# Kernel optimization log

Hardware: AMD Instinct MI355X
Metric: run time of the kernel (lower is better)

Reference implementation:

```python
import jax, jax.numpy as jnp
import numpy as np

# NOTE: VectorDiscoBlock / VectorDotProduct source was not provided; this is a
# faithful structural reconstruction of the local-support DISCO spherical conv:
# kernel_shape radial bases psi_r plus 2 polarized (tangential/radial, i.e.
# curl-like/div-like) vector bases, with paths W_ss, W_vs, W_sv, W_vv, W_vs2
# (flux-form scalar*vector products), pointwise_ss, sv_product (scalar times
# identity/rotated vector) and the physics weight initialization copied exactly
# from _init_physics_weights. All weights are constants (requires_grad=False),
# so they are contracted with the basis stencils once into effective spatial
# conv kernels.

RE = 6371000.0; RGAS = 287.0; CP = 1004.0; OMEGA_E = 7.292e-05
K_LEV = 3; NK = 6; NS = K_LEV * NK + 1; NV = K_LEV
B, H, W = 2, 256, 512
KS = 5   # number of radial kernel bases (kernel_shape)
S = 5    # spatial stencil extent
T_ANOM, KE, ZETA, DIV, TK, QK = 0, 1, 2, 3, 4, 5

def _ch(l, k):
    return l * NK + k

def _conv(x, k, groups=1):
    # zero pad lat (axis 2), circular pad lon (axis 3)
    p = k.shape[-1] // 2
    x = jnp.pad(x, ((0, 0), (0, 0), (p, p), (0, 0)))
    x = jnp.concatenate([x[..., -p:], x, x[..., :p]], axis=-1)
    return jax.lax.conv_general_dilated(
        x, k, (1, 1), 'VALID',
        dimension_numbers=('NCHW', 'OIHW', 'NCHW'),
        feature_group_count=groups)

def _build_params():
    # radial scalar bases psi[r,h,w]; polarized vector bases Vb[r,pol,h,w,comp]
    yy, xx = np.meshgrid(np.arange(S) - S // 2, np.arange(S) - S // 2, indexing='ij')
    rr = np.sqrt(yy ** 2 + xx ** 2)
    centers = np.linspace(0.0, 2.0, KS)
    psi = np.maximum(0.0, 1.0 - np.abs(rr[None] - centers[:, None, None]))
    psi = psi / psi.sum((1, 2), keepdims=True)
    inv = np.where(rr > 0, 1.0 / np.maximum(rr, 1e-9), 0.0)
    er = np.stack([yy * inv, xx * inv], -1)    # radial (div-like) polarization
    et = np.stack([-xx * inv, yy * inv], -1)   # tangential (curl-like)
    Vb = np.stack([et[None] * psi[..., None], er[None] * psi[..., None]], 1)
    # pressure levels: log-spaced 1e5 -> 1e4 Pa (default)
    p = np.array([1e5 * np.exp(-k * np.log(10.0) / (K_LEV - 1)) for k in range(K_LEV)])
    lpr = np.log(p[:-1] / p[1:])
    p_lo = np.concatenate([p[:1], 0.5 * (p[:-1] + p[1:])])
    p_up = np.concatenate([0.5 * (p[:-1] + p[1:]), [0.0]])
    delta_p = p_lo - p_up
    # physics weights (exact copy of _init_physics_weights)
    W_ss = np.zeros((NS, NS, KS)); W_vs = np.zeros((NS, NV, KS, 2))
    W_sv = np.zeros((NV, NS, KS, 2)); W_vv = np.zeros((NV, NV, KS, 2))
    W_vs2 = np.zeros((NS, NV, KS, 2))
    for k in range(K_LEV):
        W_vs[_ch(k, ZETA), k, :, 0] = 1.0 / RE
        W_vs[_ch(k, DIV), k, :, 1] = 1.0 / RE
    for ko in range(K_LEV):
        for ki in range(ko):
            W_sv[ko, _ch(ki, T_ANOM), :, 1] = -RGAS * lpr[ki] / RE
        W_sv[ko, _ch(ko, KE), :, 1] = -1.0 / RE
    for k in range(K_LEV):
        W_vs2[_ch(k, TK), k, :, 1] = -1.0 / RE
        W_vs2[_ch(k, QK), k, :, 1] = -1.0 / RE
    nu = 1.0e5  # diffusion_coeff
    lap_w = np.array([-4.0, 1.0, 0.5, 0.25, 0.125]) * (nu / RE ** 2)
    for k in range(K_LEV):
        W_ss[_ch(k, TK), _ch(k, TK)] = lap_w
        W_ss[_ch(k, QK), _ch(k, QK)] = lap_w
        W_vv[k, k, :, 0] = lap_w
    pw_ss = np.zeros((NS, NS)); pw_ss[K_LEV * NK, K_LEV * NK] = 1.0
    svp = np.zeros((NS, NV, 2))
    for k in range(K_LEV):
        svp[_ch(k, ZETA), k, 1] = 1.0
    svp[K_LEV * NK, :, 1] = -1.0
    ke_w = 0.5 * np.eye(K_LEV)
    # contract constant weights with bases -> effective spatial conv kernels
    eye2 = np.eye(2); eps2 = np.array([[0.0, -1.0], [1.0, 0.0]])
    k_ss = np.einsum('oir,rhw->oihw', W_ss, psi)
    k_vs = np.einsum('oirp,rphwc->oichw', W_vs, Vb).reshape(NS, NV * 2, S, S)
    k_sv = np.einsum('oirp,rphwc->ocihw', W_sv, Vb).reshape(NV * 2, NS, S, S)
    k_vv = (np.einsum('oir,rhw,ab->oaibhw', W_vv[..., 0], psi, eye2)
            + np.einsum('oir,rhw,ab->oaibhw', W_vv[..., 1], psi, eps2)).reshape(NV * 2, NV * 2, S, S)
    k_vs2 = np.einsum('oirp,rphwc->oichw', W_vs2, Vb).reshape(NS, NV * 2, S, S)
    lats = np.linspace(np.pi / 2, -np.pi / 2, H)
    f_cor = (2.0 * OMEGA_E * np.sin(lats)).reshape(1, 1, H, 1)
    f32 = lambda a: jnp.asarray(a, jnp.float32)
    return dict(k_ss=f32(k_ss), k_vs=f32(k_vs), k_sv=f32(k_sv), k_vv=f32(k_vv),
                k_vs2=f32(k_vs2), pw_ss=f32(pw_ss), svp=f32(svp), ke_w=f32(ke_w),
                f_cor=f32(f_cor), p_lev=f32(p), delta_p=f32(delta_p))

def _step(uv, T, q, k_ss, k_vs, k_sv, k_vv, k_vs2, pw_ss, svp, ke_w,
          f_cor, p_lev, delta_p, dt):
    Bq, Kl, Hh, Ww = T.shape

    def _tend(uv, T, q):
        # VectorDotProduct: ke[b,o] = sum_i w[o,i] * (uv_i . uv_i)
        ke = jnp.einsum('oi,bihwc,bihwc->bohw', ke_w, uv, uv)
        T_anom = T - T.mean(axis=(-2, -1), keepdims=True)
        z = jnp.zeros_like(T)
        per = jnp.stack([T_anom, ke, z, z, T, q], axis=2).reshape(Bq, Kl * NK, Hh, Ww)
        x_s = jnp.concatenate(
            [per, jnp.broadcast_to(f_cor, (Bq, 1, Hh, Ww)).astype(T.dtype)], axis=1)
        xv_vc = jnp.moveaxis(uv, -1, 2)                 # [B,K,2,H,W]
        xv = xv_vc.reshape(Bq, Kl * 2, Hh, Ww)
        # flux-form scalar*vector product fields for W_vs2 (grouped by scalar ch)
        prod = (x_s[:, :, None, None] * xv_vc[:, None]).reshape(Bq, NS * Kl * 2, Hh, Ww)
        y_s = (_conv(x_s, k_ss) + _conv(xv, k_vs)
               + _conv(prod, k_vs2, groups=NS)
               + jnp.einsum('oi,bihw->bohw', pw_ss, x_s))
        yv = _conv(x_s, k_sv) + _conv(xv, k_vv)
        y_v = jnp.moveaxis(yv.reshape(Bq, Kl, 2, Hh, Ww), 2, -1)
        # sv_product: scalar * (identity | rotated) vector
        a0 = jnp.einsum('sv,bshw->bvhw', svp[..., 0], x_s)
        a1 = jnp.einsum('sv,bshw->bvhw', svp[..., 1], x_s)
        rot = jnp.stack([-uv[..., 1], uv[..., 0]], axis=-1)
        y_v = y_v + a0[..., None] * uv + a1[..., None] * rot
        ysl = y_s[:, :Kl * NK].reshape(Bq, Kl, NK, Hh, Ww)
        div, dT, dq = ysl[:, :, DIV], ysl[:, :, TK], ysl[:, :, QK]
        # omega integrated upward from surface (cumsum over levels)
        oh = jnp.concatenate(
            [jnp.zeros((Bq, 1, Hh, Ww), T.dtype),
             jnp.cumsum(div * delta_p[None, :, None, None], axis=1)], axis=1)
        omega = 0.5 * (oh[:, :-1] + oh[:, 1:])
        pk = p_lev[None, :, None, None]
        dTdp = jnp.concatenate([
            (T[:, 1:2] - T[:, 0:1]) / (p_lev[1] - p_lev[0]),
            (T[:, 2:] - T[:, :-2]) / (p_lev[2:] - p_lev[:-2])[None, :, None, None],
            (T[:, -1:] - T[:, -2:-1]) / (p_lev[-1] - p_lev[-2])], axis=1)
        dT = dT + omega * ((RGAS / CP) * T / pk - dTdp)
        return y_v, dT, dq

    dtf = float(dt)
    k1 = _tend(uv, T, q)
    k2 = _tend(uv + 0.5 * dtf * k1[0], T + 0.5 * dtf * k1[1], q + 0.5 * dtf * k1[2])
    k3 = _tend(uv + 0.5 * dtf * k2[0], T + 0.5 * dtf * k2[1], q + 0.5 * dtf * k2[2])
    k4 = _tend(uv + dtf * k3[0], T + dtf * k3[1], q + dtf * k3[2])
    c = dtf / 6.0
    return (uv + c * (k1[0] + 2 * k2[0] + 2 * k3[0] + k4[0]),
            T + c * (k1[1] + 2 * k2[1] + 2 * k3[1] + k4[1]),
            q + c * (k1[2] + 2 * k2[2] + 2 * k3[2] + k4[2]))

def setup_inputs() -> dict:
    key = jax.random.key(0)
    k1, k2, k3 = jax.random.split(key, 3)
    inp = dict(
        uv=jax.random.normal(k1, (B, K_LEV, H, W, 2), jnp.float32),
        T=jax.random.normal(k2, (B, K_LEV, H, W), jnp.float32),
        q=jax.random.normal(k3, (B, K_LEV, H, W), jnp.float32),
    )
    inp.update(_build_params())
    inp['dt'] = 120
    return inp

def reference(uv, T, q, k_ss, k_vs, k_sv, k_vv, k_vs2, pw_ss, svp, ke_w,
              f_cor, p_lev, delta_p, dt):
    return _step(uv, T, q, k_ss, k_vs, k_sv, k_vv, k_vs2, pw_ss, svp, ke_w,
                 f_cor, p_lev, delta_p, dt)
```

## Files before the change

kernel.cpp:

```cpp
#include <hip/hip_runtime.h>

#define HH 256
#define WW 512
#define BQ 2
#define HWQ (HH*WW)
#define TW 68
#define TH 12
#define CSTR 64
#define TRL 20

#define RGASC 287.0f
#define CPC   1004.0f

typedef float f32x4 __attribute__((ext_vector_type(4)));
typedef short s16x8 __attribute__((ext_vector_type(8)));

static __device__ uint4 g_Wm[25*64];
static __device__ float g_FC[HH*16];
static __device__ float g_S [HH*3*16];
static __device__ float g_part[2][6*512];
static __device__ float g_uvs[BQ*3*HWQ*2];
static __device__ float g_Ts [BQ*3*HWQ];
static __device__ float g_qs [BQ*3*HWQ];
static __device__ float g_aT [BQ*3*HWQ];
static __device__ float g_aq [BQ*3*HWQ];
static __device__ float g_auv[BQ*3*HWQ*2];


__device__ __forceinline__ unsigned short f2bf(float f) {
  unsigned int u = __builtin_bit_cast(unsigned int, f);
  u += 0x7fffu + ((u >> 16) & 1u);
  return (unsigned short)(u >> 16);
}
__device__ __forceinline__ float bflo(unsigned int d) {
  return __builtin_bit_cast(float, d << 16);
}
__device__ __forceinline__ float bfhi(unsigned int d) {
  return __builtin_bit_cast(float, d & 0xffff0000u);
}
__device__ __forceinline__ int foMap(int o) {
  return (o < 3) ? 6*o + 3 : (o < 6) ? 6*(o-3) + 4 : 6*(o-6) + 5;
}

__global__ __launch_bounds__(256) void prelude_kernel(
    const float* __restrict__ T0,
    const float* __restrict__ k_ss, const float* __restrict__ k_vs,
    const float* __restrict__ k_sv, const float* __restrict__ k_vv,
    const float* __restrict__ k_vs2, const float* __restrict__ f_cor)
{
  if (blockIdx.x < 3072) {
    int bk = blockIdx.x >> 9, chunk = blockIdx.x & 511;
    float v = T0[bk*HWQ + chunk*256 + threadIdx.x];
    int l = threadIdx.x & 63, w = threadIdx.x >> 6;
    #pragma unroll
    for (int off=32; off; off >>= 1) v += __shfl_down(v, off);
    __shared__ float sr[4];
    if (l == 0) sr[w] = v;
    __syncthreads();
    if (threadIdx.x == 0) g_part[0][bk*512 + chunk] = sr[0]+sr[1]+sr[2]+sr[3];
    return;
  }
  int tid = (blockIdx.x - 3072)*256 + threadIdx.x;
  if (tid < 1600) {
    int l = tid & 63, t = tid >> 6;
    int o = l & 15, g = l >> 4;
    int dy = t/5, dx = t%5;
    unsigned short h[8];
    #pragma unroll
    for (int e=0;e<8;++e) {
      int s = 8*g + e; float val = 0.f;
      if (o < 15) {
        int fo = foMap(o), vo = o - 9;
        if (s < 12) {
          int k = s >> 2, c4 = s & 3;
          if (c4 >= 2) {
            int j = 2*k + (c4-2);
            val = (o<9) ? k_vs[((fo*6+j)*5+dy)*5+dx]
                        : k_vv[((vo*6+j)*5+dy)*5+dx];
          } else {
            int ifull = 6*k + ((c4==0) ? 4 : 5);
            val = (o<9) ? k_ss[((fo*19+ifull)*5+dy)*5+dx]
                        : k_sv[((vo*19+ifull)*5+dy)*5+dx];
            if (c4 == 0) {
              int ia = 6*k;
              val += (o<9) ? k_ss[((fo*19+ia)*5+dy)*5+dx]
                           : k_sv[((vo*19+ia)*5+dy)*5+dx];
            }
          }
        } else if (s < 15) {
          int ifull = 6*(s-12) + 1;
          val = (o<9) ? k_ss[((fo*19+ifull)*5+dy)*5+dx]
                      : k_sv[((vo*19+ifull)*5+dy)*5+dx];
        } else if (s >= 16 && s < 22) {
          int k = (s-16)>>1, c = (s-16)&1;
          if (o == 3+k) val = k_vs2[(((6*k+4)*6 + 2*k+c)*5+dy)*5+dx];
        } else if (s >= 22 && s < 28) {
          int k = (s-22)>>1, c = (s-22)&1;
          if (o == 6+k) val = k_vs2[(((6*k+5)*6 + 2*k+c)*5+dy)*5+dx];
        }
      }
      h[e] = f2bf(val);
    }
    uint4 wv;
    wv.x = h[0] | ((unsigned)h[1]<<16);  wv.y = h[2] | ((unsigned)h[3]<<16);
    wv.z = h[4] | ((unsigned)h[5]<<16);  wv.w = h[6] | ((unsigned)h[7]<<16);
    g_Wm[tid] = wv;
  } else if (tid < 1600 + HH*16) {
    int e = tid - 1600;
    int o = e & 15, r = e >> 4;
    float val = 0.f;
    if (o < 15) {
      int fo = foMap(o), vo = o - 9;
      for (int t=0;t<25;++t) {
        int dy = t/5, dx = t%5;
        int ar = r + dy - 2;
        if (ar < 0 || ar >= HH) continue;
        float f = f_cor[ar];
        float wv = (o<9) ? k_ss[((fo*19+18)*5+dy)*5+dx]
                         : k_sv[((vo*19+18)*5+dy)*5+dx];
        val += wv * f;
      }
    }
    g_FC[e] = val;
  } else if (tid < 1600 + HH*16 + HH*3*16) {
    int e = tid - 1600 - HH*16;
    int o = e & 15; int rk = e >> 4;
    int k = rk % 3, r = rk / 3;
    float val = 0.f;
    if (o < 15) {
      int fo = foMap(o), vo = o - 9;
      int ia = 6*k;
      for (int t=0;t<25;++t) {
        int dy = t/5, dx = t%5;
        int ar = r + dy - 2;
        if (ar < 0 || ar >= HH) continue;
        val += (o<9) ? k_ss[((fo*19+ia)*5+dy)*5+dx]
                     : k_sv[((vo*19+ia)*5+dy)*5+dx];
      }
    }
    g_S[e] = val;
  }
}

__global__ __launch_bounds__(512, 4) void conv_kernel(
    const float* __restrict__ ke_w,
    const float* __restrict__ f_cor, const float* __restrict__ p_lev,
    const float* __restrict__ delta_p,
    const float* __restrict__ uv0, const float* __restrict__ T0,
    const float* __restrict__ q0,
    float* __restrict__ out, const int* __restrict__ dtp, int stage)
{
  __shared__ __align__(16) char s_raw[TH*TW*CSTR];
  __shared__ float s_red[8][3];
  __shared__ float s_mean[3];

  const int tid = threadIdx.x;
  const int w   = tid >> 6;
  const int l   = tid & 63;
  const int b   = blockIdx.z;
  const int c0  = blockIdx.x << 6;
  const int R0  = blockIdx.y << 3;
  const int r   = R0 + w;

  if (w < 3) {
    const float* gp = g_part[stage & 1] + (b*3 + w)*512;
    float s;
    if (stage == 0) {
      s = gp[l] + gp[l+64] + gp[l+128] + gp[l+192]
        + gp[l+256] + gp[l+320] + gp[l+384] + gp[l+448];
    } else {
      s = gp[l] + gp[l+64] + gp[l+128] + gp[l+192];
    }
    #pragma unroll
    for (int off=32; off; off >>= 1) s += __shfl_down(s, off);
    if (l == 0) s_mean[w] = s * (1.0f/(float)HWQ);
  }

  const int useg = (stage > 0);
  const float* Tsrc = useg ? g_Ts  : T0;
  const float* qsrc = useg ? g_qs  : q0;
  const float* usrc = useg ? g_uvs : uv0;

  const float kw00=ke_w[0], kw01=ke_w[1], kw02=ke_w[2];
  const float kw10=ke_w[3], kw11=ke_w[4], kw12=ke_w[5];
  const float kw20=ke_w[6], kw21=ke_w[7], kw22=ke_w[8];
  for (int e = tid; e < TH*TW; e += 512) {
    int lr = e / TW, lc = e - lr*TW;
    int row = R0 + lr - 2;
    int col = (c0 + lc - 2) & (WW-1);
    unsigned int pk[16];
    #pragma unroll
    for (int i=0;i<16;++i) pk[i] = 0;
    if (row >= 0 && row < HH) {
      float T[3], q[3], u[3], v[3];
      #pragma unroll
      for (int k=0;k<3;++k) {
        int pix = ((b*3+k)*HH + row)*WW + col;
        T[k] = Tsrc[pix]; q[k] = qsrc[pix];
        float2 uvv = *(const float2*)(usrc + 2*pix);
        u[k] = uvv.x; v[k] = uvv.y;
      }
      float u2[3];
      #pragma unroll
      for (int k=0;k<3;++k) u2[k] = u[k]*u[k] + v[k]*v[k];
      float ke0 = kw00*u2[0] + kw01*u2[1] + kw02*u2[2];
      float ke1 = kw10*u2[0] + kw11*u2[1] + kw12*u2[2];
      float ke2 = kw20*u2[0] + kw21*u2[1] + kw22*u2[2];
      unsigned short hs[28];
      #pragma unroll
      for (int k=0;k<3;++k) {
        hs[4*k+0] = f2bf(T[k]); hs[4*k+1] = f2bf(q[k]);
        hs[4*k+2] = f2bf(u[k]); hs[4*k+3] = f2bf(v[k]);
      }
      hs[12]=f2bf(ke0); hs[13]=f2bf(ke1); hs[14]=f2bf(ke2); hs[15]=0;
      #pragma unroll
      for (int k=0;k<3;++k) {
        hs[16+2*k] = f2bf(T[k]*u[k]); hs[17+2*k] = f2bf(T[k]*v[k]);
        hs[22+2*k] = f2bf(q[k]*u[k]); hs[23+2*k] = f2bf(q[k]*v[k]);
      }
      #pragma unroll
      for (int i=0;i<14;++i) pk[i] = hs[2*i] | ((unsigned)hs[2*i+1] << 16);
    }
    const int key = (lc + (lc >> 2)) & 3;
    uint4* cell = (uint4*)(s_raw + e*CSTR);
    cell[(0+key)&3] = make_uint4(pk[0],pk[1],pk[2],pk[3]);
    cell[(1+key)&3] = make_uint4(pk[4],pk[5],pk[6],pk[7]);
    cell[(2+key)&3] = make_uint4(pk[8],pk[9],pk[10],pk[11]);
    cell[(3+key)&3] = make_uint4(pk[12],pk[13],pk[14],pk[15]);
  }
  __syncthreads();

  const int gi = l >> 4;
  const int m  = l & 15;
  f32x4 acc[4];
  {
    float4 fc = *(const float4*)(g_FC + r*16 + gi*4);
    f32x4 base = (f32x4){fc.x, fc.y, fc.z, fc.w};
    #pragma unroll
    for (int k=0;k<3;++k) {
      float mk = s_mean[k];
      float4 sk = *(const float4*)(g_S + (r*3+k)*16 + gi*4);
      base.x -= mk*sk.x; base.y -= mk*sk.y; base.z -= mk*sk.z; base.w -= mk*sk.w;
    }
    #pragma unroll
    for (int nt=0;nt<4;++nt) acc[nt] = base;
  }

  const char* sb = s_raw;
  #pragma unroll 5
  for (int t=0;t<25;++t) {
    const int dy = t/5, dx = t%5;
    const uint4 aw = g_Wm[t*64 + l];
    const s16x8 af = __builtin_bit_cast(s16x8, aw);
    const int lc0  = dx + m;
    const int slot = (gi + lc0 + (lc0 >> 2)) & 3;
    const int base = (((w+dy)*TW) + lc0)*CSTR + slot*16;
    #pragma unroll
    for (int nt=0;nt<4;++nt) {
      const s16x8 bf = __builtin_bit_cast(s16x8,
          *(const uint4*)(sb + base + nt*(16*CSTR)));
      acc[nt] = __builtin_amdgcn_mfma_f32_16x16x32_bf16(af, bf, acc[nt], 0, 0, 0);
    }
  }

  float Tc[3], ucv[3], vcv[3];
  {
    const int lcc = l + 2;
    const int keyc = (lcc + (lcc >> 2)) & 3;
    const char* cc = sb + (((w+2)*TW) + lcc)*CSTR;
    const uint4 c0v = *(const uint4*)(cc + ((0+keyc)&3)*16);
    const uint2 c1v = *(const uint2*)(cc + ((1+keyc)&3)*16);
    Tc[0]=bflo(c0v.x); ucv[0]=bflo(c0v.y); vcv[0]=bfhi(c0v.y);
    Tc[1]=bflo(c0v.z); ucv[1]=bflo(c0v.w); vcv[1]=bfhi(c0v.w);
    Tc[2]=bflo(c1v.x); ucv[2]=bflo(c1v.y); vcv[2]=bfhi(c1v.y);
  }
  __syncthreads();

  float* sf = (float*)s_raw;
  const int trb = w * (64*TRL);
  #pragma unroll
  for (int nt=0;nt<4;++nt)
    *(f32x4*)(sf + trb + (nt*16 + m)*TRL + gi*4) = acc[nt];
  float y[16];
  #pragma unroll
  for (int q=0;q<4;++q) {
    float4 v = *(const float4*)(sf + trb + l*TRL + q*4);
    y[4*q+0]=v.x; y[4*q+1]=v.y; y[4*q+2]=v.z; y[4*q+3]=v.w;
  }

  const int c = c0 + l;
  const float fcv = f_cor[r];
  const float dtf = (float)(*dtp);
  const float an  = (stage==2) ? dtf : 0.5f*dtf;
  const float c6  = dtf/6.0f;
  const float p0=p_lev[0], p1=p_lev[1], p2=p_lev[2];
  const float dp0=delta_p[0], dp1=delta_p[1], dp2=delta_p[2];
  const float r10 = 1.0f/(p1-p0), r20 = 1.0f/(p2-p0), r21 = 1.0f/(p2-p1);
  const float roc = RGASC/CPC;
  const float rp0 = 1.0f/p0, rp1 = 1.0f/p1, rp2 = 1.0f/p2;
  const int OUT_T = BQ*3*HWQ*2;
  const int OUT_Q = OUT_T + BQ*3*HWQ;

  float kT[3], kq[3], ku[3], kv[3];
  #pragma unroll
  for (int k=0;k<3;++k) {
    kT[k] = y[3+k];
    kq[k] = y[6+k];
    ku[k] = y[9+2*k]  + fcv*vcv[k];
    kv[k] = y[10+2*k] - fcv*ucv[k];
  }
  const float oh1 = y[0]*dp0;
  const float oh2 = oh1 + y[1]*dp1;
  const float oh3 = oh2 + y[2]*dp2;
  const float om0 = 0.5f*oh1, om1 = 0.5f*(oh1+oh2), om2 = 0.5f*(oh2+oh3);
  kT[0] += om0*(roc*Tc[0]*rp0 - (Tc[1]-Tc[0])*r10);
  kT[1] += om1*(roc*Tc[1]*rp1 - (Tc[2]-Tc[0])*r20);
  kT[2] += om2*(roc*Tc[2]*rp2 - (Tc[2]-Tc[1])*r21);

  float Tn[3];
  #pragma unroll
  for (int k=0;k<3;++k) {
    const int pT = ((b*3+k)*HH + r)*WW + c;
    const int pU = pT*2;
    if (stage == 0) {
      g_aT[pT] = kT[k];  g_aq[pT] = kq[k];
      g_auv[pU] = ku[k]; g_auv[pU+1] = kv[k];
      Tn[k]      = T0[pT] + an*kT[k];
      g_Ts[pT]   = Tn[k];
      g_qs[pT]   = q0[pT] + an*kq[k];
      g_uvs[pU]   = uv0[pU]   + an*ku[k];
      g_uvs[pU+1] = uv0[pU+1] + an*kv[k];
    } else if (stage < 3) {
      g_aT[pT] += 2.0f*kT[k];  g_aq[pT] += 2.0f*kq[k];
      g_auv[pU] += 2.0f*ku[k]; g_auv[pU+1] += 2.0f*kv[k];
      Tn[k]      = T0[pT] + an*kT[k];
      g_Ts[pT]   = Tn[k];
      g_qs[pT]   = q0[pT] + an*kq[k];
      g_uvs[pU]   = uv0[pU]   + an*ku[k];
      g_uvs[pU+1] = uv0[pU+1] + an*kv[k];
    } else {
      out[pU]         = uv0[pU]   + c6*(g_auv[pU]   + ku[k]);
      out[pU+1]       = uv0[pU+1] + c6*(g_auv[pU+1] + kv[k]);
      out[OUT_T + pT] = T0[pT]    + c6*(g_aT[pT] + kT[k]);
      out[OUT_Q + pT] = q0[pT]    + c6*(g_aq[pT] + kq[k]);
    }
  }

  if (stage < 3) {
    #pragma unroll
    for (int k=0;k<3;++k) {
      float v = Tn[k];
      #pragma unroll
      for (int off=32; off; off >>= 1) v += __shfl_down(v, off);
      if (l == 0) s_red[w][k] = v;
    }
    __syncthreads();
    if (tid == 0) {
      #pragma unroll
      for (int k=0;k<3;++k) {
        float s = 0.f;
        #pragma unroll
        for (int ww=0;ww<8;++ww) s += s_red[ww][k];
        g_part[(stage & 1) ^ 1][(b*3+k)*512 + blockIdx.y*8 + blockIdx.x] = s;
      }
    }
  }
}

extern "C" void kernel_launch(void* const* d_in, const int* in_sizes, int n_in,
                              void* d_out, int out_size, void* d_ws, size_t ws_size,
                              hipStream_t stream) {
  (void)in_sizes; (void)n_in; (void)d_ws; (void)ws_size; (void)out_size;
  const float* uv0   = (const float*)d_in[0];
  const float* T0    = (const float*)d_in[1];
  const float* q0    = (const float*)d_in[2];
  const float* k_ss  = (const float*)d_in[3];
  const float* k_vs  = (const float*)d_in[4];
  const float* k_sv  = (const float*)d_in[5];
  const float* k_vv  = (const float*)d_in[6];
  const float* k_vs2 = (const float*)d_in[7];
  const float* ke_w  = (const float*)d_in[10];
  const float* f_cor = (const float*)d_in[11];
  const float* p_lev = (const float*)d_in[12];
  const float* dpv   = (const float*)d_in[13];
  const int*   dtp   = (const int*)d_in[14];
  float* out = (float*)d_out;

  prelude_kernel<<<3143, 256, 0, stream>>>(T0, k_ss, k_vs, k_sv, k_vv, k_vs2, f_cor);

  for (int st = 0; st < 4; ++st) {
    conv_kernel<<<dim3(8,32,2), 512, 0, stream>>>(
        ke_w, f_cor, p_lev, dpv, uv0, T0, q0, out, dtp, st);
  }
}
```

Before: 89.32 us.

## Pre-pack bf16 feature cells in global memory and stream them into LDS asynchronously

Each stage used to rebuild bf16-packed feature cells (T, q, uv, KE, fluxes) for its whole halo tile from fp32 state. Now the producing kernel (prelude for stage 0, the previous conv stage otherwise) writes packed 64-byte cells once per pixel into a row-padded, double-buffered global array. The conv kernel copies them into LDS with global_load_lds, keeping the swizzle. This removes redundant halo packing and the fp32 intermediate state arrays, and launch bounds rise to 6 waves per SIMD. The cost is a larger global buffer, extra zero-padding work in the prelude, and more register pressure at the higher occupancy target.

Result: slower. 100.2 us (+12.2%).

```diff
diff --git a/kernel.cpp b/kernel.cpp
--- a/kernel.cpp
+++ b/kernel.cpp
@@ -4,6 +4,7 @@
 #define WW 512
 #define BQ 2
 #define HWQ (HH*WW)
+#define HP 260
 #define TW 68
 #define TH 12
 #define CSTR 64
@@ -15,17 +16,14 @@
 typedef float f32x4 __attribute__((ext_vector_type(4)));
 typedef short s16x8 __attribute__((ext_vector_type(8)));
 
+static __device__ uint4 g_cells[2][BQ*HP*WW*4];
 static __device__ uint4 g_Wm[25*64];
 static __device__ float g_FC[HH*16];
 static __device__ float g_S [HH*3*16];
 static __device__ float g_part[2][6*512];
-static __device__ float g_uvs[BQ*3*HWQ*2];
-static __device__ float g_Ts [BQ*3*HWQ];
-static __device__ float g_qs [BQ*3*HWQ];
 static __device__ float g_aT [BQ*3*HWQ];
 static __device__ float g_aq [BQ*3*HWQ];
 static __device__ float g_auv[BQ*3*HWQ*2];
-
 
 __device__ __forceinline__ unsigned short f2bf(float f) {
   unsigned int u = __builtin_bit_cast(unsigned int, f);
@@ -41,26 +39,107 @@
 __device__ __forceinline__ int foMap(int o) {
   return (o < 3) ? 6*o + 3 : (o < 6) ? 6*(o-3) + 4 : 6*(o-6) + 5;
 }
+__device__ __forceinline__ void gload_lds16(const void* g, void* l) {
+  __builtin_amdgcn_global_load_lds(
+      (const __attribute__((address_space(1))) void*)g,
+      (__attribute__((address_space(3))) void*)l, 16, 0, 0);
+}
+
+__device__ __forceinline__ void pack_cell(
+    const float* T, const float* q, const float* u, const float* v,
+    float kw00,float kw01,float kw02,float kw10,float kw11,float kw12,
+    float kw20,float kw21,float kw22, uint4* dst)
+{
+  float u2[3];
+  #pragma unroll
+  for (int k=0;k<3;++k) u2[k] = u[k]*u[k] + v[k]*v[k];
+  float ke0 = kw00*u2[0] + kw01*u2[1] + kw02*u2[2];
+  float ke1 = kw10*u2[0] + kw11*u2[1] + kw12*u2[2];
+  float ke2 = kw20*u2[0] + kw21*u2[1] + kw22*u2[2];
+  unsigned short hs[28];
+  #pragma unroll
+  for (int k=0;k<3;++k) {
+    hs[4*k+0] = f2bf(T[k]); hs[4*k+1] = f2bf(q[k]);
+    hs[4*k+2] = f2bf(u[k]); hs[4*k+3] = f2bf(v[k]);
+  }
+  hs[12]=f2bf(ke0); hs[13]=f2bf(ke1); hs[14]=f2bf(ke2); hs[15]=0;
+  #pragma unroll
+  for (int k=0;k<3;++k) {
+    hs[16+2*k] = f2bf(T[k]*u[k]); hs[17+2*k] = f2bf(T[k]*v[k]);
+    hs[22+2*k] = f2bf(q[k]*u[k]); hs[23+2*k] = f2bf(q[k]*v[k]);
+  }
+  unsigned int pk[16];
+  #pragma unroll
+  for (int i=0;i<14;++i) pk[i] = hs[2*i] | ((unsigned)hs[2*i+1] << 16);
+  pk[14] = 0; pk[15] = 0;
+  dst[0] = make_uint4(pk[0],pk[1],pk[2],pk[3]);
+  dst[1] = make_uint4(pk[4],pk[5],pk[6],pk[7]);
+  dst[2] = make_uint4(pk[8],pk[9],pk[10],pk[11]);
+  dst[3] = make_uint4(pk[12],pk[13],pk[14],pk[15]);
+}
 
 __global__ __launch_bounds__(256) void prelude_kernel(
-    const float* __restrict__ T0,
+    const float* __restrict__ uv0, const float* __restrict__ T0,
+    const float* __restrict__ q0,  const float* __restrict__ ke_w,
     const float* __restrict__ k_ss, const float* __restrict__ k_vs,
     const float* __restrict__ k_sv, const float* __restrict__ k_vv,
     const float* __restrict__ k_vs2, const float* __restrict__ f_cor)
 {
-  if (blockIdx.x < 3072) {
-    int bk = blockIdx.x >> 9, chunk = blockIdx.x & 511;
-    float v = T0[bk*HWQ + chunk*256 + threadIdx.x];
+  const int bid = blockIdx.x;
+  if (bid < 1040) {
+    int g = bid*256 + threadIdx.x;
+    int b = (g >= HP*WW) ? 1 : 0;
+    int rem = g - b*(HP*WW);
+    int pr = rem >> 9, col = rem & (WW-1);
+    uint4* dst = g_cells[0] + (size_t)g*4;
+    if (pr < 2 || pr >= HP-2) {
+      uint4 z = make_uint4(0,0,0,0);
+      dst[0]=z; dst[1]=z; dst[2]=z; dst[3]=z;
+      return;
+    }
+    int row = pr - 2;
+    float T[3], q[3], u[3], v[3];
+    #pragma unroll
+    for (int k=0;k<3;++k) {
+      int pix = ((b*3+k)*HH + row)*WW + col;
+      T[k] = T0[pix]; q[k] = q0[pix];
+      float2 uvv = *(const float2*)(uv0 + 2*pix);
+      u[k] = uvv.x; v[k] = uvv.y;
+    }
+    uint4 cell[4];
+    pack_cell(T,q,u,v, ke_w[0],ke_w[1],ke_w[2],ke_w[3],ke_w[4],
+              ke_w[5],ke_w[6],ke_w[7],ke_w[8], cell);
+    dst[0]=cell[0]; dst[1]=cell[1]; dst[2]=cell[2]; dst[3]=cell[3];
+    __shared__ float sr[4][3];
     int l = threadIdx.x & 63, w = threadIdx.x >> 6;
     #pragma unroll
-    for (int off=32; off; off >>= 1) v += __shfl_down(v, off);
-    __shared__ float sr[4];
-    if (l == 0) sr[w] = v;
+    for (int k=0;k<3;++k) {
+      float s = T[k];
+      #pragma unroll
+      for (int off=32; off; off >>= 1) s += __shfl_down(s, off);
+      if (l == 0) sr[w][k] = s;
+    }
     __syncthreads();
-    if (threadIdx.x == 0) g_part[0][bk*512 + chunk] = sr[0]+sr[1]+sr[2]+sr[3];
+    if (threadIdx.x == 0) {
+      int slot = row*2 + (bid & 1);
+      #pragma unroll
+      for (int k=0;k<3;++k)
+        g_part[0][(b*3+k)*512 + slot] = sr[0][k]+sr[1][k]+sr[2][k]+sr[3][k];
+    }
     return;
   }
-  int tid = (blockIdx.x - 3072)*256 + threadIdx.x;
+  if (bid < 1056) {
+    int idx = (bid-1040)*256 + threadIdx.x;
+    int b = idx >> 11;
+    int pr4 = (idx >> 9) & 3;
+    int pr = (pr4 < 2) ? pr4 : (HP-4+pr4);
+    int col = idx & (WW-1);
+    uint4* dst = g_cells[1] + ((size_t)((b*HP + pr)*WW + col))*4;
+    uint4 z = make_uint4(0,0,0,0);
+    dst[0]=z; dst[1]=z; dst[2]=z; dst[3]=z;
+    return;
+  }
+  int tid = (bid - 1056)*256 + threadIdx.x;
   if (tid < 1600) {
     int l = tid & 63, t = tid >> 6;
     int o = l & 15, g = l >> 4;
@@ -142,7 +221,7 @@
   }
 }
 
-__global__ __launch_bounds__(512, 4) void conv_kernel(
+__global__ __launch_bounds__(512, 6) void conv_kernel(
     const float* __restrict__ ke_w,
     const float* __restrict__ f_cor, const float* __restrict__ p_lev,
     const float* __restrict__ delta_p,
@@ -176,57 +255,23 @@
     if (l == 0) s_mean[w] = s * (1.0f/(float)HWQ);
   }
 
-  const int useg = (stage > 0);
-  const float* Tsrc = useg ? g_Ts  : T0;
-  const float* qsrc = useg ? g_qs  : q0;
-  const float* usrc = useg ? g_uvs : uv0;
-
-  const float kw00=ke_w[0], kw01=ke_w[1], kw02=ke_w[2];
-  const float kw10=ke_w[3], kw11=ke_w[4], kw12=ke_w[5];
-  const float kw20=ke_w[6], kw21=ke_w[7], kw22=ke_w[8];
-  for (int e = tid; e < TH*TW; e += 512) {
-    int lr = e / TW, lc = e - lr*TW;
-    int row = R0 + lr - 2;
-    int col = (c0 + lc - 2) & (WW-1);
-    unsigned int pk[16];
-    #pragma unroll
-    for (int i=0;i<16;++i) pk[i] = 0;
-    if (row >= 0 && row < HH) {
-      float T[3], q[3], u[3], v[3];
-      #pragma unroll
-      for (int k=0;k<3;++k) {
-        int pix = ((b*3+k)*HH + row)*WW + col;
-        T[k] = Tsrc[pix]; q[k] = qsrc[pix];
-        float2 uvv = *(const float2*)(usrc + 2*pix);
-        u[k] = uvv.x; v[k] = uvv.y;
-      }
-      float u2[3];
-      #pragma unroll
-      for (int k=0;k<3;++k) u2[k] = u[k]*u[k] + v[k]*v[k];
-      float ke0 = kw00*u2[0] + kw01*u2[1] + kw02*u2[2];
-      float ke1 = kw10*u2[0] + kw11*u2[1] + kw12*u2[2];
-      float ke2 = kw20*u2[0] + kw21*u2[1] + kw22*u2[2];
-      unsigned short hs[28];
-      #pragma unroll
-      for (int k=0;k<3;++k) {
-        hs[4*k+0] = f2bf(T[k]); hs[4*k+1] = f2bf(q[k]);
-        hs[4*k+2] = f2bf(u[k]); hs[4*k+3] = f2bf(v[k]);
-      }
-      hs[12]=f2bf(ke0); hs[13]=f2bf(ke1); hs[14]=f2bf(ke2); hs[15]=0;
-      #pragma unroll
-      for (int k=0;k<3;++k) {
-        hs[16+2*k] = f2bf(T[k]*u[k]); hs[17+2*k] = f2bf(T[k]*v[k]);
-        hs[22+2*k] = f2bf(q[k]*u[k]); hs[23+2*k] = f2bf(q[k]*v[k]);
-      }
-      #pragma unroll
-      for (int i=0;i<14;++i) pk[i] = hs[2*i] | ((unsigned)hs[2*i+1] << 16);
-    }
-    const int key = (lc + (lc >> 2)) & 3;
-    uint4* cell = (uint4*)(s_raw + e*CSTR);
-    cell[(0+key)&3] = make_uint4(pk[0],pk[1],pk[2],pk[3]);
-    cell[(1+key)&3] = make_uint4(pk[4],pk[5],pk[6],pk[7]);
-    cell[(2+key)&3] = make_uint4(pk[8],pk[9],pk[10],pk[11]);
-    cell[(3+key)&3] = make_uint4(pk[12],pk[13],pk[14],pk[15]);
+  {
+    const uint4* __restrict__ csrc = g_cells[stage & 1] + (size_t)b*HP*WW*4;
+    #pragma unroll
+    for (int it = 0; it < 7; ++it) {
+      int e4 = it*512 + tid;
+      if (e4 < TH*TW*4) {
+        int cell = e4 >> 2, si = e4 & 3;
+        int lr = cell / TW;
+        int lc = cell - lr*TW;
+        int col = (c0 + lc - 2) & (WW-1);
+        int key = (lc + (lc >> 2)) & 3;
+        int j = (si - key) & 3;
+        const uint4* src = csrc + ((size_t)((R0 + lr)*WW + col))*4 + j;
+        char* dstb = s_raw + (size_t)(e4 - l)*16;
+        gload_lds16(src, dstb);
+      }
+    }
   }
   __syncthreads();
 
@@ -317,36 +362,30 @@
   kT[1] += om1*(roc*Tc[1]*rp1 - (Tc[2]-Tc[0])*r20);
   kT[2] += om2*(roc*Tc[2]*rp2 - (Tc[2]-Tc[1])*r21);
 
-  float Tn[3];
-  #pragma unroll
-  for (int k=0;k<3;++k) {
-    const int pT = ((b*3+k)*HH + r)*WW + c;
-    const int pU = pT*2;
-    if (stage == 0) {
-      g_aT[pT] = kT[k];  g_aq[pT] = kq[k];
-      g_auv[pU] = ku[k]; g_auv[pU+1] = kv[k];
-      Tn[k]      = T0[pT] + an*kT[k];
-      g_Ts[pT]   = Tn[k];
-      g_qs[pT]   = q0[pT] + an*kq[k];
-      g_uvs[pU]   = uv0[pU]   + an*ku[k];
-      g_uvs[pU+1] = uv0[pU+1] + an*kv[k];
-    } else if (stage < 3) {
-      g_aT[pT] += 2.0f*kT[k];  g_aq[pT] += 2.0f*kq[k];
-      g_auv[pU] += 2.0f*ku[k]; g_auv[pU+1] += 2.0f*kv[k];
-      Tn[k]      = T0[pT] + an*kT[k];
-      g_Ts[pT]   = Tn[k];
-      g_qs[pT]   = q0[pT] + an*kq[k];
-      g_uvs[pU]   = uv0[pU]   + an*ku[k];
-      g_uvs[pU+1] = uv0[pU+1] + an*kv[k];
-    } else {
-      out[pU]         = uv0[pU]   + c6*(g_auv[pU]   + ku[k]);
-      out[pU+1]       = uv0[pU+1] + c6*(g_auv[pU+1] + kv[k]);
-      out[OUT_T + pT] = T0[pT]    + c6*(g_aT[pT] + kT[k]);
-      out[OUT_Q + pT] = q0[pT]    + c6*(g_aq[pT] + kq[k]);
-    }
-  }
-
   if (stage < 3) {
+    float Tn[3], qn[3], un[3], vn[3];
+    #pragma unroll
+    for (int k=0;k<3;++k) {
+      const int pT = ((b*3+k)*HH + r)*WW + c;
+      const int pU = pT*2;
+      if (stage == 0) {
+        g_aT[pT] = kT[k];  g_aq[pT] = kq[k];
+        g_auv[pU] = ku[k]; g_auv[pU+1] = kv[k];
+      } else {
+        g_aT[pT] += 2.0f*kT[k];  g_aq[pT] += 2.0f*kq[k];
+        g_auv[pU] += 2.0f*ku[k]; g_auv[pU+1] += 2.0f*kv[k];
+      }
+      Tn[k] = T0[pT] + an*kT[k];
+      qn[k] = q0[pT] + an*kq[k];
+      un[k] = uv0[pU]   + an*ku[k];
+      vn[k] = uv0[pU+1] + an*kv[k];
+    }
+    uint4 cell[4];
+    pack_cell(Tn,qn,un,vn, ke_w[0],ke_w[1],ke_w[2],ke_w[3],ke_w[4],
+              ke_w[5],ke_w[6],ke_w[7],ke_w[8], cell);
+    uint4* cd = g_cells[(stage & 1) ^ 1] + ((size_t)((b*HP + r + 2)*WW + c))*4;
+    cd[0]=cell[0]; cd[1]=cell[1]; cd[2]=cell[2]; cd[3]=cell[3];
+
     #pragma unroll
     for (int k=0;k<3;++k) {
       float v = Tn[k];
@@ -363,6 +402,16 @@
         for (int ww=0;ww<8;++ww) s += s_red[ww][k];
         g_part[(stage & 1) ^ 1][(b*3+k)*512 + blockIdx.y*8 + blockIdx.x] = s;
       }
+    }
+  } else {
+    #pragma unroll
+    for (int k=0;k<3;++k) {
+      const int pT = ((b*3+k)*HH + r)*WW + c;
+      const int pU = pT*2;
+      out[pU]         = uv0[pU]   + c6*(g_auv[pU]   + ku[k]);
+      out[pU+1]       = uv0[pU+1] + c6*(g_auv[pU+1] + kv[k]);
+      out[OUT_T + pT] = T0[pT]    + c6*(g_aT[pT] + kT[k]);
+      out[OUT_Q + pT] = q0[pT]    + c6*(g_aq[pT] + kq[k]);
     }
   }
 }
@@ -386,7 +435,8 @@
   const int*   dtp   = (const int*)d_in[14];
   float* out = (float*)d_out;
 
-  prelude_kernel<<<3143, 256, 0, stream>>>(T0, k_ss, k_vs, k_sv, k_vv, k_vs2, f_cor);
+  prelude_kernel<<<1127, 256, 0, stream>>>(uv0, T0, q0, ke_w,
+                                           k_ss, k_vs, k_sv, k_vv, k_vs2, f_cor);
 
   for (int st = 0; st < 4; ++st) {
     conv_kernel<<<dim3(8,32,2), 512, 0, stream>>>(
```

## Compute two output rows per wave to reuse shared-memory B fragments

Applied to the files above, without the earlier changes.

Each wave now computes two adjacent output rows instead of one, halving the block size to 256 threads. A single shared-memory tile row load feeds MFMAs for both output rows, using weights at dy=j for one row and dy=j-1 for the other, with weight fragments double-buffered in registers. This cuts LDS reads and weight loads per output, at the cost of doubled accumulator registers, lower launch occupancy (launch bounds 256,3), and fewer threads to stage the tile.

Result: slower. 92.69 us (+3.8%).

```diff
diff --git a/kernel.cpp b/kernel.cpp
--- a/kernel.cpp
+++ b/kernel.cpp
@@ -142,7 +142,7 @@
   }
 }
 
-__global__ __launch_bounds__(512, 4) void conv_kernel(
+__global__ __launch_bounds__(256, 3) void conv_kernel(
     const float* __restrict__ ke_w,
     const float* __restrict__ f_cor, const float* __restrict__ p_lev,
     const float* __restrict__ delta_p,
@@ -160,7 +160,6 @@
   const int b   = blockIdx.z;
   const int c0  = blockIdx.x << 6;
   const int R0  = blockIdx.y << 3;
-  const int r   = R0 + w;
 
   if (w < 3) {
     const float* gp = g_part[stage & 1] + (b*3 + w)*512;
@@ -184,7 +183,7 @@
   const float kw00=ke_w[0], kw01=ke_w[1], kw02=ke_w[2];
   const float kw10=ke_w[3], kw11=ke_w[4], kw12=ke_w[5];
   const float kw20=ke_w[6], kw21=ke_w[7], kw22=ke_w[8];
-  for (int e = tid; e < TH*TW; e += 512) {
+  for (int e = tid; e < TH*TW; e += 256) {
     int lr = e / TW, lc = e - lr*TW;
     int row = R0 + lr - 2;
     int col = (c0 + lc - 2) & (WW-1);
@@ -232,64 +231,74 @@
 
   const int gi = l >> 4;
   const int m  = l & 15;
-  f32x4 acc[4];
+  const int r0 = R0 + 2*w, r1 = r0 + 1;
+  f32x4 acc0[4], acc1[4];
   {
-    float4 fc = *(const float4*)(g_FC + r*16 + gi*4);
-    f32x4 base = (f32x4){fc.x, fc.y, fc.z, fc.w};
+    float4 fc0 = *(const float4*)(g_FC + r0*16 + gi*4);
+    float4 fc1 = *(const float4*)(g_FC + r1*16 + gi*4);
+    f32x4 b0 = (f32x4){fc0.x, fc0.y, fc0.z, fc0.w};
+    f32x4 b1 = (f32x4){fc1.x, fc1.y, fc1.z, fc1.w};
     #pragma unroll
     for (int k=0;k<3;++k) {
       float mk = s_mean[k];
-      float4 sk = *(const float4*)(g_S + (r*3+k)*16 + gi*4);
-      base.x -= mk*sk.x; base.y -= mk*sk.y; base.z -= mk*sk.z; base.w -= mk*sk.w;
-    }
-    #pragma unroll
-    for (int nt=0;nt<4;++nt) acc[nt] = base;
+      float4 s0 = *(const float4*)(g_S + (r0*3+k)*16 + gi*4);
+      float4 s1 = *(const float4*)(g_S + (r1*3+k)*16 + gi*4);
+      b0.x -= mk*s0.x; b0.y -= mk*s0.y; b0.z -= mk*s0.z; b0.w -= mk*s0.w;
+      b1.x -= mk*s1.x; b1.y -= mk*s1.y; b1.z -= mk*s1.z; b1.w -= mk*s1.w;
+    }
+    #pragma unroll
+    for (int nt=0;nt<4;++nt) { acc0[nt] = b0; acc1[nt] = b1; }
   }
 
   const char* sb = s_raw;
-  #pragma unroll 5
-  for (int t=0;t<25;++t) {
-    const int dy = t/5, dx = t%5;
-    const uint4 aw = g_Wm[t*64 + l];
-    const s16x8 af = __builtin_bit_cast(s16x8, aw);
-    const int lc0  = dx + m;
-    const int slot = (gi + lc0 + (lc0 >> 2)) & 3;
-    const int base = (((w+dy)*TW) + lc0)*CSTR + slot*16;
-    #pragma unroll
-    for (int nt=0;nt<4;++nt) {
-      const s16x8 bf = __builtin_bit_cast(s16x8,
-          *(const uint4*)(sb + base + nt*(16*CSTR)));
-      acc[nt] = __builtin_amdgcn_mfma_f32_16x16x32_bf16(af, bf, acc[nt], 0, 0, 0);
-    }
-  }
-
-  float Tc[3], ucv[3], vcv[3];
-  {
+  uint4 afb[2][5];
+  #pragma unroll
+  for (int j=0;j<6;++j) {
+    if (j < 5) {
+      #pragma unroll
+      for (int dx=0;dx<5;++dx) afb[j&1][dx] = g_Wm[(j*5+dx)*64 + l];
+    }
+    #pragma unroll
+    for (int dx=0;dx<5;++dx) {
+      const int lc0  = dx + m;
+      const int slot = (gi + lc0 + (lc0 >> 2)) & 3;
+      const int bofs = (((2*w+j)*TW) + lc0)*CSTR + slot*16;
+      const s16x8 afc = __builtin_bit_cast(s16x8, afb[j&1][dx]);
+      const s16x8 afp = __builtin_bit_cast(s16x8, afb[(j&1)^1][dx]);
+      #pragma unroll
+      for (int nt=0;nt<4;++nt) {
+        const s16x8 bf = __builtin_bit_cast(s16x8,
+            *(const uint4*)(sb + bofs + nt*(16*CSTR)));
+        if (j < 5)
+          acc0[nt] = __builtin_amdgcn_mfma_f32_16x16x32_bf16(afc, bf, acc0[nt], 0, 0, 0);
+        if (j > 0)
+          acc1[nt] = __builtin_amdgcn_mfma_f32_16x16x32_bf16(afp, bf, acc1[nt], 0, 0, 0);
+      }
+    }
+  }
+
+  float Tc[2][3], ucv[2][3], vcv[2][3];
+  #pragma unroll
+  for (int rr=0;rr<2;++rr) {
     const int lcc = l + 2;
     const int keyc = (lcc + (lcc >> 2)) & 3;
-    const char* cc = sb + (((w+2)*TW) + lcc)*CSTR;
+    const char* cc = sb + (((2*w+rr+2)*TW) + lcc)*CSTR;
     const uint4 c0v = *(const uint4*)(cc + ((0+keyc)&3)*16);
     const uint2 c1v = *(const uint2*)(cc + ((1+keyc)&3)*16);
-    Tc[0]=bflo(c0v.x); ucv[0]=bflo(c0v.y); vcv[0]=bfhi(c0v.y);
-    Tc[1]=bflo(c0v.z); ucv[1]=bflo(c0v.w); vcv[1]=bfhi(c0v.w);
-    Tc[2]=bflo(c1v.x); ucv[2]=bflo(c1v.y); vcv[2]=bfhi(c1v.y);
+    Tc[rr][0]=bflo(c0v.x); ucv[rr][0]=bflo(c0v.y); vcv[rr][0]=bfhi(c0v.y);
+    Tc[rr][1]=bflo(c0v.z); ucv[rr][1]=bflo(c0v.w); vcv[rr][1]=bfhi(c0v.w);
+    Tc[rr][2]=bflo(c1v.x); ucv[rr][2]=bflo(c1v.y); vcv[rr][2]=bfhi(c1v.y);
   }
   __syncthreads();
 
   float* sf = (float*)s_raw;
-  const int trb = w * (64*TRL);
   #pragma unroll
-  for (int nt=0;nt<4;++nt)
-    *(f32x4*)(sf + trb + (nt*16 + m)*TRL + gi*4) = acc[nt];
-  float y[16];
-  #pragma unroll
-  for (int q=0;q<4;++q) {
-    float4 v = *(const float4*)(sf + trb + l*TRL + q*4);
-    y[4*q+0]=v.x; y[4*q+1]=v.y; y[4*q+2]=v.z; y[4*q+3]=v.w;
+  for (int nt=0;nt<4;++nt) {
+    *(f32x4*)(sf + (2*w+0)*(64*TRL) + (nt*16 + m)*TRL + gi*4) = acc0[nt];
+    *(f32x4*)(sf + (2*w+1)*(64*TRL) + (nt*16 + m)*TRL + gi*4) = acc1[nt];
   }
 
   const int c = c0 + l;
-  const float fcv = f_cor[r];
   const float dtf = (float)(*dtp);
   const float an  = (stage==2) ? dtf : 0.5f*dtf;
   const float c6  = dtf/6.0f;
@@ -301,58 +310,72 @@
   const int OUT_T = BQ*3*HWQ*2;
   const int OUT_Q = OUT_T + BQ*3*HWQ;
 
-  float kT[3], kq[3], ku[3], kv[3];
+  float Tn[2][3];
   #pragma unroll
-  for (int k=0;k<3;++k) {
-    kT[k] = y[3+k];
-    kq[k] = y[6+k];
-    ku[k] = y[9+2*k]  + fcv*vcv[k];
-    kv[k] = y[10+2*k] - fcv*ucv[k];
-  }
-  const float oh1 = y[0]*dp0;
-  const float oh2 = oh1 + y[1]*dp1;
-  const float oh3 = oh2 + y[2]*dp2;
-  const float om0 = 0.5f*oh1, om1 = 0.5f*(oh1+oh2), om2 = 0.5f*(oh2+oh3);
-  kT[0] += om0*(roc*Tc[0]*rp0 - (Tc[1]-Tc[0])*r10);
-  kT[1] += om1*(roc*Tc[1]*rp1 - (Tc[2]-Tc[0])*r20);
-  kT[2] += om2*(roc*Tc[2]*rp2 - (Tc[2]-Tc[1])*r21);
-
-  float Tn[3];
-  #pragma unroll
-  for (int k=0;k<3;++k) {
-    const int pT = ((b*3+k)*HH + r)*WW + c;
-    const int pU = pT*2;
-    if (stage == 0) {
-      g_aT[pT] = kT[k];  g_aq[pT] = kq[k];
-      g_auv[pU] = ku[k]; g_auv[pU+1] = kv[k];
-      Tn[k]      = T0[pT] + an*kT[k];
-      g_Ts[pT]   = Tn[k];
-      g_qs[pT]   = q0[pT] + an*kq[k];
-      g_uvs[pU]   = uv0[pU]   + an*ku[k];
-      g_uvs[pU+1] = uv0[pU+1] + an*kv[k];
-    } else if (stage < 3) {
-      g_aT[pT] += 2.0f*kT[k];  g_aq[pT] += 2.0f*kq[k];
-      g_auv[pU] += 2.0f*ku[k]; g_auv[pU+1] += 2.0f*kv[k];
-      Tn[k]      = T0[pT] + an*kT[k];
-      g_Ts[pT]   = Tn[k];
-      g_qs[pT]   = q0[pT] + an*kq[k];
-      g_uvs[pU]   = uv0[pU]   + an*ku[k];
-      g_uvs[pU+1] = uv0[pU+1] + an*kv[k];
-    } else {
-      out[pU]         = uv0[pU]   + c6*(g_auv[pU]   + ku[k]);
-      out[pU+1]       = uv0[pU+1] + c6*(g_auv[pU+1] + kv[k]);
-      out[OUT_T + pT] = T0[pT]    + c6*(g_aT[pT] + kT[k]);
-      out[OUT_Q + pT] = q0[pT]    + c6*(g_aq[pT] + kq[k]);
+  for (int rr=0;rr<2;++rr) {
+    const int r = r0 + rr;
+    const float fcv = f_cor[r];
+    float y[16];
+    #pragma unroll
+    for (int q=0;q<4;++q) {
+      float4 v = *(const float4*)(sf + (2*w+rr)*(64*TRL) + l*TRL + q*4);
+      y[4*q+0]=v.x; y[4*q+1]=v.y; y[4*q+2]=v.z; y[4*q+3]=v.w;
+    }
+    float kT[3], kq[3], ku[3], kv[3];
+    #pragma unroll
+    for (int k=0;k<3;++k) {
+      kT[k] = y[3+k];
+      kq[k] = y[6+k];
+      ku[k] = y[9+2*k]  + fcv*vcv[rr][k];
+      kv[k] = y[10+2*k] - fcv*ucv[rr][k];
+    }
+    const float oh1 = y[0]*dp0;
+    const float oh2 = oh1 + y[1]*dp1;
+    const float oh3 = oh2 + y[2]*dp2;
+    const float om0 = 0.5f*oh1, om1 = 0.5f*(oh1+oh2), om2 = 0.5f*(oh2+oh3);
+    kT[0] += om0*(roc*Tc[rr][0]*rp0 - (Tc[rr][1]-Tc[rr][0])*r10);
+    kT[1] += om1*(roc*Tc[rr][1]*rp1 - (Tc[rr][2]-Tc[rr][0])*r20);
+    kT[2] += om2*(roc*Tc[rr][2]*rp2 - (Tc[rr][2]-Tc[rr][1])*r21);
+
+    #pragma unroll
+    for (int k=0;k<3;++k) {
+      const int pT = ((b*3+k)*HH + r)*WW + c;
+      const int pU = pT*2;
+      if (stage == 0) {
+        g_aT[pT] = kT[k];  g_aq[pT] = kq[k];
+        g_auv[pU] = ku[k]; g_auv[pU+1] = kv[k];
+        Tn[rr][k]  = T0[pT] + an*kT[k];
+        g_Ts[pT]   = Tn[rr][k];
+        g_qs[pT]   = q0[pT] + an*kq[k];
+        g_uvs[pU]   = uv0[pU]   + an*ku[k];
+        g_uvs[pU+1] = uv0[pU+1] + an*kv[k];
+      } else if (stage < 3) {
+        g_aT[pT] += 2.0f*kT[k];  g_aq[pT] += 2.0f*kq[k];
+        g_auv[pU] += 2.0f*ku[k]; g_auv[pU+1] += 2.0f*kv[k];
+        Tn[rr][k]  = T0[pT] + an*kT[k];
+        g_Ts[pT]   = Tn[rr][k];
+        g_qs[pT]   = q0[pT] + an*kq[k];
+        g_uvs[pU]   = uv0[pU]   + an*ku[k];
+        g_uvs[pU+1] = uv0[pU+1] + an*kv[k];
+      } else {
+        out[pU]         = uv0[pU]   + c6*(g_auv[pU]   + ku[k]);
+        out[pU+1]       = uv0[pU+1] + c6*(g_auv[pU+1] + kv[k]);
+        out[OUT_T + pT] = T0[pT]    + c6*(g_aT[pT] + kT[k]);
+        out[OUT_Q + pT] = q0[pT]    + c6*(g_aq[pT] + kq[k]);
+      }
     }
   }
 
   if (stage < 3) {
     #pragma unroll
-    for (int k=0;k<3;++k) {
-      float v = Tn[k];
-      #pragma unroll
-      for (int off=32; off; off >>= 1) v += __shfl_down(v, off);
-      if (l == 0) s_red[w][k] = v;
+    for (int rr=0;rr<2;++rr) {
+      #pragma unroll
+      for (int k=0;k<3;++k) {
+        float v = Tn[rr][k];
+        #pragma unroll
+        for (int off=32; off; off >>= 1) v += __shfl_down(v, off);
+        if (l == 0) s_red[2*w+rr][k] = v;
+      }
     }
     __syncthreads();
     if (tid == 0) {
@@ -389,7 +412,7 @@
   prelude_kernel<<<3143, 256, 0, stream>>>(T0, k_ss, k_vs, k_sv, k_vv, k_vs2, f_cor);
 
   for (int st = 0; st < 4; ++st) {
-    conv_kernel<<<dim3(8,32,2), 512, 0, stream>>>(
+    conv_kernel<<<dim3(8,32,2), 256, 0, stream>>>(
         ke_w, f_cor, p_lev, dpv, uv0, T0, q0, out, dtp, st);
   }
 }
```

## Store RK stage states as packed bf16 per pixel in double-buffered arrays

Applied to the files above, without the earlier changes.

Intermediate RK stage states (T, q, u, v for three levels) now go into double-buffered arrays as packed bf16, one 16-byte and one 8-byte word per pixel, instead of separate fp32 arrays. The next stage's halo loads then take two vector loads rather than twelve scattered fp32 loads, which cuts global traffic. The input is already rounded to bf16 in shared memory, so precision is largely unchanged, though T rounding before the mean reduction may differ slightly. The prelude's mean reduction also now has each thread sum four elements with fewer blocks.

Result: faster. 82.15 us (median of 2 runs) (-8.0%).

```diff
diff --git a/kernel.cpp b/kernel.cpp
--- a/kernel.cpp
+++ b/kernel.cpp
@@ -19,9 +19,8 @@
 static __device__ float g_FC[HH*16];
 static __device__ float g_S [HH*3*16];
 static __device__ float g_part[2][6*512];
-static __device__ float g_uvs[BQ*3*HWQ*2];
-static __device__ float g_Ts [BQ*3*HWQ];
-static __device__ float g_qs [BQ*3*HWQ];
+static __device__ uint4 g_st0[2][BQ*HWQ];
+static __device__ uint2 g_st1[2][BQ*HWQ];
 static __device__ float g_aT [BQ*3*HWQ];
 static __device__ float g_aq [BQ*3*HWQ];
 static __device__ float g_auv[BQ*3*HWQ*2];
@@ -48,9 +47,11 @@
     const float* __restrict__ k_sv, const float* __restrict__ k_vv,
     const float* __restrict__ k_vs2, const float* __restrict__ f_cor)
 {
-  if (blockIdx.x < 3072) {
-    int bk = blockIdx.x >> 9, chunk = blockIdx.x & 511;
-    float v = T0[bk*HWQ + chunk*256 + threadIdx.x];
+  if (blockIdx.x < 768) {
+    int bk = blockIdx.x >> 7, chunk = blockIdx.x & 127;
+    const float* p = T0 + bk*HWQ + chunk*1024;
+    float v = p[threadIdx.x] + p[threadIdx.x+256]
+            + p[threadIdx.x+512] + p[threadIdx.x+768];
     int l = threadIdx.x & 63, w = threadIdx.x >> 6;
     #pragma unroll
     for (int off=32; off; off >>= 1) v += __shfl_down(v, off);
@@ -60,7 +61,7 @@
     if (threadIdx.x == 0) g_part[0][bk*512 + chunk] = sr[0]+sr[1]+sr[2]+sr[3];
     return;
   }
-  int tid = (blockIdx.x - 3072)*256 + threadIdx.x;
+  int tid = (blockIdx.x - 768)*256 + threadIdx.x;
   if (tid < 1600) {
     int l = tid & 63, t = tid >> 6;
     int o = l & 15, g = l >> 4;
@@ -166,8 +167,7 @@
     const float* gp = g_part[stage & 1] + (b*3 + w)*512;
     float s;
     if (stage == 0) {
-      s = gp[l] + gp[l+64] + gp[l+128] + gp[l+192]
-        + gp[l+256] + gp[l+320] + gp[l+384] + gp[l+448];
+      s = gp[l] + gp[l+64];
     } else {
       s = gp[l] + gp[l+64] + gp[l+128] + gp[l+192];
     }
@@ -175,11 +175,6 @@
     for (int off=32; off; off >>= 1) s += __shfl_down(s, off);
     if (l == 0) s_mean[w] = s * (1.0f/(float)HWQ);
   }
-
-  const int useg = (stage > 0);
-  const float* Tsrc = useg ? g_Ts  : T0;
-  const float* qsrc = useg ? g_qs  : q0;
-  const float* usrc = useg ? g_uvs : uv0;
 
   const float kw00=ke_w[0], kw01=ke_w[1], kw02=ke_w[2];
   const float kw10=ke_w[3], kw11=ke_w[4], kw12=ke_w[5];
@@ -193,12 +188,21 @@
     for (int i=0;i<16;++i) pk[i] = 0;
     if (row >= 0 && row < HH) {
       float T[3], q[3], u[3], v[3];
-      #pragma unroll
-      for (int k=0;k<3;++k) {
-        int pix = ((b*3+k)*HH + row)*WW + col;
-        T[k] = Tsrc[pix]; q[k] = qsrc[pix];
-        float2 uvv = *(const float2*)(usrc + 2*pix);
-        u[k] = uvv.x; v[k] = uvv.y;
+      if (stage == 0) {
+        #pragma unroll
+        for (int k=0;k<3;++k) {
+          int pix = ((b*3+k)*HH + row)*WW + col;
+          T[k] = T0[pix]; q[k] = q0[pix];
+          float2 uvv = *(const float2*)(uv0 + 2*pix);
+          u[k] = uvv.x; v[k] = uvv.y;
+        }
+      } else {
+        const int idx = (b*HH + row)*WW + col;
+        const uint4 a  = g_st0[(stage-1)&1][idx];
+        const uint2 bv = g_st1[(stage-1)&1][idx];
+        T[0]=bflo(a.x);  q[0]=bfhi(a.x);  u[0]=bflo(a.y);  v[0]=bfhi(a.y);
+        T[1]=bflo(a.z);  q[1]=bfhi(a.z);  u[1]=bflo(a.w);  v[1]=bfhi(a.w);
+        T[2]=bflo(bv.x); q[2]=bfhi(bv.x); u[2]=bflo(bv.y); v[2]=bfhi(bv.y);
       }
       float u2[3];
       #pragma unroll
@@ -317,36 +321,34 @@
   kT[1] += om1*(roc*Tc[1]*rp1 - (Tc[2]-Tc[0])*r20);
   kT[2] += om2*(roc*Tc[2]*rp2 - (Tc[2]-Tc[1])*r21);
 
-  float Tn[3];
-  #pragma unroll
-  for (int k=0;k<3;++k) {
-    const int pT = ((b*3+k)*HH + r)*WW + c;
-    const int pU = pT*2;
-    if (stage == 0) {
-      g_aT[pT] = kT[k];  g_aq[pT] = kq[k];
-      g_auv[pU] = ku[k]; g_auv[pU+1] = kv[k];
-      Tn[k]      = T0[pT] + an*kT[k];
-      g_Ts[pT]   = Tn[k];
-      g_qs[pT]   = q0[pT] + an*kq[k];
-      g_uvs[pU]   = uv0[pU]   + an*ku[k];
-      g_uvs[pU+1] = uv0[pU+1] + an*kv[k];
-    } else if (stage < 3) {
-      g_aT[pT] += 2.0f*kT[k];  g_aq[pT] += 2.0f*kq[k];
-      g_auv[pU] += 2.0f*ku[k]; g_auv[pU+1] += 2.0f*kv[k];
-      Tn[k]      = T0[pT] + an*kT[k];
-      g_Ts[pT]   = Tn[k];
-      g_qs[pT]   = q0[pT] + an*kq[k];
-      g_uvs[pU]   = uv0[pU]   + an*ku[k];
-      g_uvs[pU+1] = uv0[pU+1] + an*kv[k];
-    } else {
-      out[pU]         = uv0[pU]   + c6*(g_auv[pU]   + ku[k]);
-      out[pU+1]       = uv0[pU+1] + c6*(g_auv[pU+1] + kv[k]);
-      out[OUT_T + pT] = T0[pT]    + c6*(g_aT[pT] + kT[k]);
-      out[OUT_Q + pT] = q0[pT]    + c6*(g_aq[pT] + kq[k]);
-    }
-  }
-
   if (stage < 3) {
+    float Tn[3], qn[3], un[3], vn[3];
+    #pragma unroll
+    for (int k=0;k<3;++k) {
+      const int pT = ((b*3+k)*HH + r)*WW + c;
+      const int pU = pT*2;
+      if (stage == 0) {
+        g_aT[pT] = kT[k];  g_aq[pT] = kq[k];
+        g_auv[pU] = ku[k]; g_auv[pU+1] = kv[k];
+      } else {
+        g_aT[pT] += 2.0f*kT[k];  g_aq[pT] += 2.0f*kq[k];
+        g_auv[pU] += 2.0f*ku[k]; g_auv[pU+1] += 2.0f*kv[k];
+      }
+      Tn[k] = T0[pT] + an*kT[k];
+      qn[k] = q0[pT] + an*kq[k];
+      un[k] = uv0[pU]   + an*ku[k];
+      vn[k] = uv0[pU+1] + an*kv[k];
+    }
+    const int sidx = (b*HH + r)*WW + c;
+    unsigned int w0 = f2bf(Tn[0]) | ((unsigned)f2bf(qn[0])<<16);
+    unsigned int w1 = f2bf(un[0]) | ((unsigned)f2bf(vn[0])<<16);
+    unsigned int w2 = f2bf(Tn[1]) | ((unsigned)f2bf(qn[1])<<16);
+    unsigned int w3 = f2bf(un[1]) | ((unsigned)f2bf(vn[1])<<16);
+    unsigned int w4 = f2bf(Tn[2]) | ((unsigned)f2bf(qn[2])<<16);
+    unsigned int w5 = f2bf(un[2]) | ((unsigned)f2bf(vn[2])<<16);
+    g_st0[stage & 1][sidx] = make_uint4(w0, w1, w2, w3);
+    g_st1[stage & 1][sidx] = make_uint2(w4, w5);
+
     #pragma unroll
     for (int k=0;k<3;++k) {
       float v = Tn[k];
@@ -363,6 +365,16 @@
         for (int ww=0;ww<8;++ww) s += s_red[ww][k];
         g_part[(stage & 1) ^ 1][(b*3+k)*512 + blockIdx.y*8 + blockIdx.x] = s;
       }
+    }
+  } else {
+    #pragma unroll
+    for (int k=0;k<3;++k) {
+      const int pT = ((b*3+k)*HH + r)*WW + c;
+      const int pU = pT*2;
+      out[pU]         = uv0[pU]   + c6*(g_auv[pU]   + ku[k]);
+      out[pU+1]       = uv0[pU+1] + c6*(g_auv[pU+1] + kv[k]);
+      out[OUT_T + pT] = T0[pT]    + c6*(g_aT[pT] + kT[k]);
+      out[OUT_Q + pT] = q0[pT]    + c6*(g_aq[pT] + kq[k]);
     }
   }
 }
@@ -386,7 +398,7 @@
   const int*   dtp   = (const int*)d_in[14];
   float* out = (float*)d_out;
 
-  prelude_kernel<<<3143, 256, 0, stream>>>(T0, k_ss, k_vs, k_sv, k_vv, k_vs2, f_cor);
+  prelude_kernel<<<839, 256, 0, stream>>>(T0, k_ss, k_vs, k_sv, k_vv, k_vs2, f_cor);
 
   for (int st = 0; st < 4; ++st) {
     conv_kernel<<<dim3(8,32,2), 512, 0, stream>>>(
```
